# Performance work log

Measured on AMD Instinct MI355X. Metric: run time of the kernel, lower is better.

## Reference

```python
import jax, jax.numpy as jnp
import numpy as np


def setup_inputs() -> dict:
    key = jax.random.key(0)
    k1, k2 = jax.random.split(key)
    B, N, D, T = 32, 1024, 512, 4096
    x = jax.random.normal(k1, (B, N, D), dtype=jnp.float32)
    durations = jax.random.randint(k2, (B, N), 0, 8, dtype=jnp.int64)
    return {"x": x, "durations": durations, "target_len": T}


def reference(x, durations, target_len):
    """Vectorized length regulator.

    For each output frame t, the source phoneme index is
    searchsorted(cumsum(durations), t, side='right'): frame t belongs to
    phoneme i iff csum[i-1] <= t < csum[i]. This replaces the per-batch
    repeat_interleave loop with a single gather.
    """
    B, N, D = x.shape
    T = target_len
    dur = durations.astype(jnp.int32)
    csum = jnp.cumsum(dur, axis=1)           # (B, N)
    total = csum[:, -1]                       # (B,) valid frames per batch
    t = jnp.arange(T, dtype=jnp.int32)        # (T,)
    # per-batch frame -> phoneme index
    idx = jax.vmap(lambda c: jnp.searchsorted(c, t, side='right'))(csum)  # (B, T)
    mask = t[None, :] < total[:, None]        # (B, T)
    idx_c = jnp.clip(idx, 0, N - 1)
    gathered = jnp.take_along_axis(x, idx_c[:, :, None], axis=1)  # (B, T, D)
    expanded = jnp.where(mask[:, :, None], gathered, jnp.zeros((), x.dtype))
    return expanded, mask
```

## Files before the change

### kernel.cpp

```cpp
#include <hip/hip_runtime.h>

#define B_ 32
#define N_ 1024
#define D_ 512
#define T_ 4096
#define D4_ (D_ / 4)

typedef float f4_t __attribute__((ext_vector_type(4)));

__global__ __launch_bounds__(N_) void lr_scan_kernel(
    const int* __restrict__ dur,
    int* __restrict__ idxmap,
    float* __restrict__ mask_out)
{
    __shared__ int wsum[16];
    const int b = blockIdx.x;
    const int tid = threadIdx.x;
    const int lane = tid & 63;
    const int wave = tid >> 6;

    const int d = dur[b * N_ + tid];

    int v = d;
#pragma unroll
    for (int off = 1; off < 64; off <<= 1) {
        int u = __shfl_up(v, off, 64);
        if (lane >= off) v += u;
    }
    if (lane == 63) wsum[wave] = v;
    __syncthreads();

    if (tid < 16) {
        int w = wsum[tid];
#pragma unroll
        for (int off = 1; off < 16; off <<= 1) {
            int u = __shfl_up(w, off, 16);
            if (tid >= off) w += u;
        }
        wsum[tid] = w;
    }
    __syncthreads();

    const int end   = v + (wave ? wsum[wave - 1] : 0);
    const int start = end - d;
    const int total = wsum[15];

    const int cs = min(start, T_);
    const int ce = min(end,   T_);
    for (int t = cs; t < ce; ++t) {
        idxmap[b * T_ + t] = tid;
    }

    for (int t = total + tid; t < T_; t += N_) {
        idxmap[b * T_ + t] = -1;
    }

    for (int t = tid; t < T_; t += N_) {
        mask_out[b * T_ + t] = (t < total) ? 1.0f : 0.0f;
    }
}

__global__ __launch_bounds__(256) void lr_gather_kernel(
    const f4_t* __restrict__ x,
    const int* __restrict__ idxmap,
    f4_t* __restrict__ out)
{
    const int base = blockIdx.x * 1024 + threadIdx.x;
#pragma unroll
    for (int k = 0; k < 4; ++k) {
        const int gid   = base + k * 256;
        const int frame = gid >> 7;
        const int idx   = __builtin_amdgcn_readfirstlane(idxmap[frame]);
        f4_t val = (f4_t){0.f, 0.f, 0.f, 0.f};
        if (idx >= 0) {
            const int b = frame >> 12;
            val = x[(b * N_ + idx) * D4_ + (gid & (D4_ - 1))];
        }
        __builtin_nontemporal_store(val, &out[gid]);
    }
}

extern "C" void kernel_launch(void* const* d_in, const int* in_sizes, int n_in,
                              void* d_out, int out_size, void* d_ws, size_t ws_size,
                              hipStream_t stream) {
    const float* x   = (const float*)d_in[0];
    const int*   dur = (const int*)d_in[1];

    float* out      = (float*)d_out;
    float* mask_out = out + (size_t)B_ * T_ * D_;
    int*   idxmap   = (int*)d_ws;

    lr_scan_kernel<<<B_, N_, 0, stream>>>(dur, idxmap, mask_out);

    const int total4 = B_ * T_ * D4_;
    lr_gather_kernel<<<total4 / 1024, 256, 0, stream>>>(
        (const f4_t*)x, idxmap, (f4_t*)out);
}
```

Measured before the change: 312.8 us.

## Expand per phoneme: read each x row once and broadcast to its frames

The scan kernel now writes per-phoneme cumulative sums instead of a per-frame index map. The expand kernel assigns one wave per source phoneme, loads that row of x once into registers, and stores it repeatedly to every output frame it covers. The tail frames past the total length are zero-filled by striding over phonemes. This removes the idxmap write/read and the redundant x reloads, at the cost of load imbalance across waves (durations 0..7) and dropping the nontemporal stores.

```diff
diff --git a/kernel.cpp b/kernel.cpp
--- a/kernel.cpp
+++ b/kernel.cpp
@@ -10,7 +10,7 @@
 
 __global__ __launch_bounds__(N_) void lr_scan_kernel(
     const int* __restrict__ dur,
-    int* __restrict__ idxmap,
+    int* __restrict__ csum,
     float* __restrict__ mask_out)
 {
     __shared__ int wsum[16];
@@ -42,41 +42,49 @@
     __syncthreads();
 
     const int end   = v + (wave ? wsum[wave - 1] : 0);
-    const int start = end - d;
     const int total = wsum[15];
 
-    const int cs = min(start, T_);
-    const int ce = min(end,   T_);
-    for (int t = cs; t < ce; ++t) {
-        idxmap[b * T_ + t] = tid;
-    }
-
-    for (int t = total + tid; t < T_; t += N_) {
-        idxmap[b * T_ + t] = -1;
-    }
+    csum[b * N_ + tid] = end;
 
     for (int t = tid; t < T_; t += N_) {
         mask_out[b * T_ + t] = (t < total) ? 1.0f : 0.0f;
     }
 }
 
-__global__ __launch_bounds__(256) void lr_gather_kernel(
+__global__ __launch_bounds__(256) void lr_expand_kernel(
     const f4_t* __restrict__ x,
-    const int* __restrict__ idxmap,
+    const int* __restrict__ csum,
     f4_t* __restrict__ out)
 {
-    const int base = blockIdx.x * 1024 + threadIdx.x;
-#pragma unroll
-    for (int k = 0; k < 4; ++k) {
-        const int gid   = base + k * 256;
-        const int frame = gid >> 7;
-        const int idx   = __builtin_amdgcn_readfirstlane(idxmap[frame]);
-        f4_t val = (f4_t){0.f, 0.f, 0.f, 0.f};
-        if (idx >= 0) {
-            const int b = frame >> 12;
-            val = x[(b * N_ + idx) * D4_ + (gid & (D4_ - 1))];
+    const int wid  = (blockIdx.x * 256 + threadIdx.x) >> 6;
+    const int lane = threadIdx.x & 63;
+    const int b = wid >> 10;
+    const int i = wid & (N_ - 1);
+
+    const int end   = csum[b * N_ + i];
+    const int start = i ? csum[b * N_ + i - 1] : 0;
+    const int total = csum[b * N_ + N_ - 1];
+
+    const int cs = min(start, T_);
+    const int ce = min(end,   T_);
+
+    if (cs < ce) {
+        const f4_t* xrow = x + (size_t)(b * N_ + i) * D4_;
+        const f4_t lo = xrow[lane];
+        const f4_t hi = xrow[lane + 64];
+        f4_t* orow = out + ((size_t)b * T_ + cs) * D4_;
+        for (int t = cs; t < ce; ++t) {
+            orow[lane]      = lo;
+            orow[lane + 64] = hi;
+            orow += D4_;
         }
-        __builtin_nontemporal_store(val, &out[gid]);
+    }
+
+    const f4_t z = (f4_t){0.f, 0.f, 0.f, 0.f};
+    for (int t = total + i; t < T_; t += N_) {
+        f4_t* orow = out + ((size_t)b * T_ + t) * D4_;
+        orow[lane]      = z;
+        orow[lane + 64] = z;
     }
 }
 
@@ -88,11 +96,10 @@
 
     float* out      = (float*)d_out;
     float* mask_out = out + (size_t)B_ * T_ * D_;
-    int*   idxmap   = (int*)d_ws;
+    int*   csum     = (int*)d_ws;
 
-    lr_scan_kernel<<<B_, N_, 0, stream>>>(dur, idxmap, mask_out);
+    lr_scan_kernel<<<B_, N_, 0, stream>>>(dur, csum, mask_out);
 
-    const int total4 = B_ * T_ * D4_;
-    lr_gather_kernel<<<total4 / 1024, 256, 0, stream>>>(
-        (const f4_t*)x, idxmap, (f4_t*)out);
+    lr_expand_kernel<<<(B_ * N_) / 4, 256, 0, stream>>>(
+        (const f4_t*)x, csum, (f4_t*)out);
 }
```

After: 323.5 us. 1.03x slower.
